# Kernel tuning notes

Measured on AMD Instinct MI355X. Metric: run time of the kernel, lower is better.

Reference implementation:

```python
import jax, jax.numpy as jnp
import numpy as np

N = 50000
E = 800000
IN_C = 128
HID = 64
HEADS = 4
OUT_C = 1
NEG_SLOPE = 0.2  # PyG GATConv default


def setup_inputs() -> dict:
    key = jax.random.key(0)
    ks = jax.random.split(key, 12)
    s = 1.0 / np.sqrt(IN_C)
    s2 = 1.0 / np.sqrt(HEADS * HID)
    return {
        "x": jax.random.normal(ks[0], (N, IN_C), jnp.float32),
        "edge_index": jax.random.randint(ks[1], (2, E), 0, N, jnp.int64),
        # layer 1 params (heads=HEADS, concat=True)
        "W1": jax.random.normal(ks[2], (IN_C, HEADS * HID), jnp.float32) * s,
        "att_src1": jax.random.normal(ks[3], (HEADS, HID), jnp.float32) * s,
        "att_dst1": jax.random.normal(ks[4], (HEADS, HID), jnp.float32) * s,
        "b1": jnp.zeros((HEADS * HID,), jnp.float32),
        # layer 2 params (heads=1, concat=False)
        "W2": jax.random.normal(ks[5], (HEADS * HID, OUT_C), jnp.float32) * s2,
        "att_src2": jax.random.normal(ks[6], (1, OUT_C), jnp.float32) * s2,
        "att_dst2": jax.random.normal(ks[7], (1, OUT_C), jnp.float32) * s2,
        "b2": jnp.zeros((OUT_C,), jnp.float32),
    }


def _gat_layer(x, src, dst, W, att_src, att_dst, b, concat):
    heads, out_c = att_src.shape
    h = (x @ W).reshape(-1, heads, out_c)          # [N, H, F]
    # per-node attention scores, gathered per edge (scalars, cheap)
    s_src = jnp.einsum('nhf,hf->nh', h, att_src)   # [N, H]
    s_dst = jnp.einsum('nhf,hf->nh', h, att_dst)
    e = jax.nn.leaky_relu(s_src[src] + s_dst[dst], NEG_SLOPE)  # [E, H]
    # segment softmax over edges sharing a destination
    m = jax.ops.segment_max(e, dst, num_segments=N)            # [N, H]
    m = jnp.where(jnp.isfinite(m), m, 0.0)
    ex = jnp.exp(e - m[dst])
    denom = jax.ops.segment_sum(ex, dst, num_segments=N)       # [N, H]
    alpha = ex / denom[dst]                                    # [E, H]
    # weighted scatter-aggregate of source features
    agg = jax.ops.segment_sum(alpha[:, :, None] * h[src], dst, num_segments=N)  # [N, H, F]
    out = agg.reshape(-1, heads * out_c) if concat else agg.mean(axis=1)
    return out + b


def reference(x, edge_index, W1, att_src1, att_dst1, b1, W2, att_src2, att_dst2, b2):
    # PyG GATConv default: add self loops
    loop = jnp.arange(N, dtype=edge_index.dtype)
    src = jnp.concatenate([edge_index[0], loop])
    dst = jnp.concatenate([edge_index[1], loop])
    h = _gat_layer(x, src, dst, W1, att_src1, att_dst1, b1, concat=True)
    h = jax.nn.elu(h)
    return _gat_layer(h, src, dst, W2, att_src2, att_dst2, b2, concat=False)
```

## Files before the change

kernel.cpp:

```cpp
#include <hip/hip_runtime.h>
#include <math.h>

#define NN 50000
#define EE 800000
#define ETOT 850000
#define NEG 0.2f
#define CAP 64

typedef unsigned short ushort_t;
typedef __attribute__((ext_vector_type(8))) short bf16x8;
typedef __attribute__((ext_vector_type(4))) float f32x4;

__device__ __forceinline__ float bf2f(ushort_t u) {
    return __uint_as_float((unsigned)u << 16);
}
__device__ __forceinline__ ushort_t f2bf(float f) {
    unsigned u = __float_as_uint(f);
    unsigned r = (u + 0x7FFFu + ((u >> 16) & 1u)) >> 16;
    return (ushort_t)r;
}

__global__ void k_detect(const void* ei, int* flag) {
    if (threadIdx.x == 0) {
        const long long* p = (const long long*)ei;
        int ok = 1;
        for (int i = 0; i < 64; ++i) {
            long long v = p[i];
            if (v < 0 || v >= NN) ok = 0;
        }
        *flag = ok;
    }
}

__device__ __forceinline__ int load_idx(const void* ei, int f64, long long pos) {
    return f64 ? (int)((const long long*)ei)[pos] : ((const int*)ei)[pos];
}

__global__ void k_fill(const void* ei, const int* __restrict__ flag,
                       int* cursor, int* __restrict__ esrc) {
    int e = blockIdx.x * blockDim.x + threadIdx.x;
    if (e >= ETOT) return;
    int f = *flag;
    int src, dst;
    if (e < EE) {
        src = load_idx(ei, f, e);
        dst = load_idx(ei, f, (long long)EE + e);
    } else {
        src = dst = e - EE;
    }
    int pos = atomicAdd(&cursor[dst], 1);
    if (pos < CAP) esrc[dst * CAP + pos] = src;
}

__global__ __launch_bounds__(256) void k_wprep(const float* __restrict__ W,
                                               ushort_t* __restrict__ Wf) {
    int idx = blockIdx.x * 256 + threadIdx.x;
    int e = idx & 7, l = (idx >> 3) & 63, ct = (idx >> 9) & 15, kt = idx >> 13;
    int k = kt * 32 + (l >> 4) * 8 + e;
    int col = ct * 16 + (l & 15);
    Wf[idx] = f2bf(W[k * 256 + col]);
}

__device__ __forceinline__ bf16x8 cvt8(float4 a, float4 b) {
    bf16x8 v;
    v[0] = (short)f2bf(a.x); v[1] = (short)f2bf(a.y);
    v[2] = (short)f2bf(a.z); v[3] = (short)f2bf(a.w);
    v[4] = (short)f2bf(b.x); v[5] = (short)f2bf(b.y);
    v[6] = (short)f2bf(b.z); v[7] = (short)f2bf(b.w);
    return v;
}

__global__ __launch_bounds__(256) void k_gemm_mfma(
    const float* __restrict__ x, const ushort_t* __restrict__ Wf,
    const float* __restrict__ aS, const float* __restrict__ aD,
    ushort_t* __restrict__ h1b, float* __restrict__ sS, float* __restrict__ sD) {
    int t = threadIdx.x, wid = t >> 6, l = t & 63;
    int lg = l >> 4, lr = l & 15;
    int r0 = blockIdx.x * 32;
    int c0 = wid * 64;
    int rowA0 = r0 + lr;       if (rowA0 >= NN) rowA0 = NN - 1;
    int rowA1 = r0 + 16 + lr;  if (rowA1 >= NN) rowA1 = NN - 1;
    const float4* X0 = (const float4*)(x + (size_t)rowA0 * 128) + lg * 2;
    const float4* X1 = (const float4*)(x + (size_t)rowA1 * 128) + lg * 2;
    const bf16x8* Bv = (const bf16x8*)Wf;

    f32x4 acc[2][4] = {};
#pragma unroll
    for (int kt = 0; kt < 4; ++kt) {
        bf16x8 a0 = cvt8(X0[kt * 8], X0[kt * 8 + 1]);
        bf16x8 a1 = cvt8(X1[kt * 8], X1[kt * 8 + 1]);
#pragma unroll
        for (int ct = 0; ct < 4; ++ct) {
            bf16x8 b = Bv[(size_t)((kt * 16 + wid * 4 + ct) * 64 + l)];
            acc[0][ct] = __builtin_amdgcn_mfma_f32_16x16x32_bf16(a0, b, acc[0][ct], 0, 0, 0);
            acc[1][ct] = __builtin_amdgcn_mfma_f32_16x16x32_bf16(a1, b, acc[1][ct], 0, 0, 0);
        }
    }
    float aSl[4], aDl[4];
#pragma unroll
    for (int ct = 0; ct < 4; ++ct) {
        aSl[ct] = aS[c0 + ct * 16 + lr];
        aDl[ct] = aD[c0 + ct * 16 + lr];
    }
#pragma unroll
    for (int rt = 0; rt < 2; ++rt) {
#pragma unroll
        for (int q = 0; q < 4; ++q) {
            int row = r0 + rt * 16 + lg * 4 + q;
            bool ok = row < NN;
            float p = 0.f, dd = 0.f;
#pragma unroll
            for (int ct = 0; ct < 4; ++ct) {
                float v = acc[rt][ct][q];
                if (ok) h1b[(size_t)row * 256 + c0 + ct * 16 + lr] = f2bf(v);
                p = fmaf(v, aSl[ct], p);
                dd = fmaf(v, aDl[ct], dd);
            }
#pragma unroll
            for (int k = 8; k >= 1; k >>= 1) {
                p += __shfl_xor(p, k, 64);
                dd += __shfl_xor(dd, k, 64);
            }
            if (ok && lr == 0) {
                sS[row * 4 + wid] = p;
                sD[row * 4 + wid] = dd;
            }
        }
    }
}

__global__ __launch_bounds__(256) void k_agg1(
    const int* __restrict__ cursor, const int* __restrict__ esrc,
    const ushort_t* __restrict__ h1b, const float* __restrict__ sS,
    const float* __restrict__ sD, const float* __restrict__ b1,
    const float* __restrict__ W2, float* __restrict__ g) {
    __shared__ float4 e_lds[4][CAP];
    __shared__ int s_lds[4][CAP];
    int wid = threadIdx.x >> 6, lane = threadIdx.x & 63;
    int n = blockIdx.x * 4 + wid;
    if (n >= NN) return;
    int d = cursor[n];
    if (d > CAP) d = CAP;
    int dp = (d + 3) & ~3;
    float sd0 = sD[n * 4 + 0], sd1 = sD[n * 4 + 1];
    float sd2 = sD[n * 4 + 2], sd3 = sD[n * 4 + 3];
    float e0 = -1e30f, e1 = -1e30f, e2 = -1e30f, e3 = -1e30f;
    int s = 0;
    if (lane < d) {
        s = esrc[n * CAP + lane];
        float4 ss = *(const float4*)(sS + (size_t)s * 4);
        e0 = ss.x + sd0; e0 = e0 > 0.f ? e0 : NEG * e0;
        e1 = ss.y + sd1; e1 = e1 > 0.f ? e1 : NEG * e1;
        e2 = ss.z + sd2; e2 = e2 > 0.f ? e2 : NEG * e2;
        e3 = ss.w + sd3; e3 = e3 > 0.f ? e3 : NEG * e3;
    }
    if (lane < dp) {
        e_lds[wid][lane] = make_float4(e0, e1, e2, e3);
        s_lds[wid][lane] = s;
    }
    float m0 = e0, m1 = e1, m2 = e2, m3 = e3;
#pragma unroll
    for (int k = 32; k >= 1; k >>= 1) {
        m0 = fmaxf(m0, __shfl_xor(m0, k, 64));
        m1 = fmaxf(m1, __shfl_xor(m1, k, 64));
        m2 = fmaxf(m2, __shfl_xor(m2, k, 64));
        m3 = fmaxf(m3, __shfl_xor(m3, k, 64));
    }
    float a0 = 0, a1 = 0, a2 = 0, a3 = 0;
    float d0 = 0, d1 = 0, d2 = 0, d3 = 0;
    for (int j = 0; j < dp; j += 4) {
        float4 ev0 = e_lds[wid][j + 0];
        float4 ev1 = e_lds[wid][j + 1];
        float4 ev2 = e_lds[wid][j + 2];
        float4 ev3 = e_lds[wid][j + 3];
        int s0 = s_lds[wid][j + 0];
        int s1 = s_lds[wid][j + 1];
        int s2 = s_lds[wid][j + 2];
        int s3 = s_lds[wid][j + 3];
        const ushort_t* h0 = h1b + (size_t)s0 * 256 + lane;
        const ushort_t* h1 = h1b + (size_t)s1 * 256 + lane;
        const ushort_t* h2 = h1b + (size_t)s2 * 256 + lane;
        const ushort_t* h3 = h1b + (size_t)s3 * 256 + lane;
        ushort_t u00 = h0[0], u01 = h0[64], u02 = h0[128], u03 = h0[192];
        ushort_t u10 = h1[0], u11 = h1[64], u12 = h1[128], u13 = h1[192];
        ushort_t u20 = h2[0], u21 = h2[64], u22 = h2[128], u23 = h2[192];
        ushort_t u30 = h3[0], u31 = h3[64], u32 = h3[128], u33 = h3[192];
        float x00 = __expf(ev0.x - m0), x01 = __expf(ev0.y - m1);
        float x02 = __expf(ev0.z - m2), x03 = __expf(ev0.w - m3);
        float x10 = __expf(ev1.x - m0), x11 = __expf(ev1.y - m1);
        float x12 = __expf(ev1.z - m2), x13 = __expf(ev1.w - m3);
        float x20 = __expf(ev2.x - m0), x21 = __expf(ev2.y - m1);
        float x22 = __expf(ev2.z - m2), x23 = __expf(ev2.w - m3);
        float x30 = __expf(ev3.x - m0), x31 = __expf(ev3.y - m1);
        float x32 = __expf(ev3.z - m2), x33 = __expf(ev3.w - m3);
        d0 += (x00 + x10) + (x20 + x30);
        d1 += (x01 + x11) + (x21 + x31);
        d2 += (x02 + x12) + (x22 + x32);
        d3 += (x03 + x13) + (x23 + x33);
        a0 = fmaf(x00, bf2f(u00), a0); a0 = fmaf(x10, bf2f(u10), a0);
        a0 = fmaf(x20, bf2f(u20), a0); a0 = fmaf(x30, bf2f(u30), a0);
        a1 = fmaf(x01, bf2f(u01), a1); a1 = fmaf(x11, bf2f(u11), a1);
        a1 = fmaf(x21, bf2f(u21), a1); a1 = fmaf(x31, bf2f(u31), a1);
        a2 = fmaf(x02, bf2f(u02), a2); a2 = fmaf(x12, bf2f(u12), a2);
        a2 = fmaf(x22, bf2f(u22), a2); a2 = fmaf(x32, bf2f(u32), a2);
        a3 = fmaf(x03, bf2f(u03), a3); a3 = fmaf(x13, bf2f(u13), a3);
        a3 = fmaf(x23, bf2f(u23), a3); a3 = fmaf(x33, bf2f(u33), a3);
    }
    float o0 = a0 / d0 + b1[lane];
    float o1 = a1 / d1 + b1[64 + lane];
    float o2 = a2 / d2 + b1[128 + lane];
    float o3 = a3 / d3 + b1[192 + lane];
    o0 = o0 > 0.f ? o0 : expm1f(o0);
    o1 = o1 > 0.f ? o1 : expm1f(o1);
    o2 = o2 > 0.f ? o2 : expm1f(o2);
    o3 = o3 > 0.f ? o3 : expm1f(o3);
    float part = o0 * W2[lane] + o1 * W2[64 + lane] + o2 * W2[128 + lane] + o3 * W2[192 + lane];
#pragma unroll
    for (int k = 32; k >= 1; k >>= 1) part += __shfl_xor(part, k, 64);
    if (lane == 0) g[n] = part;
}

__global__ __launch_bounds__(256) void k_layer2(
    const int* __restrict__ cursor, const int* __restrict__ esrc,
    const float* __restrict__ g, const float* __restrict__ aS2,
    const float* __restrict__ aD2, const float* __restrict__ b2,
    float* __restrict__ out) {
    int wid = threadIdx.x >> 6, lane = threadIdx.x & 63;
    int n = blockIdx.x * 4 + wid;
    if (n >= NN) return;
    int d = cursor[n];
    if (d > CAP) d = CAP;
    float aS = aS2[0], aD = aD2[0];
    float dn = g[n] * aD;
    float gv = 0.f, e = -1e30f;
    if (lane < d) {
        gv = g[esrc[n * CAP + lane]];
        e = gv * aS + dn;
        e = e > 0.f ? e : NEG * e;
    }
    float m = e;
#pragma unroll
    for (int k = 32; k >= 1; k >>= 1) m = fmaxf(m, __shfl_xor(m, k, 64));
    float ex = (lane < d) ? __expf(e - m) : 0.f;
    float den = ex, ws = ex * gv;
#pragma unroll
    for (int k = 32; k >= 1; k >>= 1) {
        den += __shfl_xor(den, k, 64);
        ws += __shfl_xor(ws, k, 64);
    }
    if (lane == 0) out[n] = ws / den + b2[0];
}

extern "C" void kernel_launch(void* const* d_in, const int* in_sizes, int n_in,
                              void* d_out, int out_size, void* d_ws, size_t ws_size,
                              hipStream_t stream) {
    const float* x   = (const float*)d_in[0];
    const void*  ei  = d_in[1];
    const float* W1  = (const float*)d_in[2];
    const float* aS1 = (const float*)d_in[3];
    const float* aD1 = (const float*)d_in[4];
    const float* b1  = (const float*)d_in[5];
    const float* W2  = (const float*)d_in[6];
    const float* aS2 = (const float*)d_in[7];
    const float* aD2 = (const float*)d_in[8];
    const float* b2  = (const float*)d_in[9];
    float* out = (float*)d_out;

    char* w = (char*)d_ws;
    size_t off = 0;
    auto take = [&](size_t bytes) {
        char* p = w + off;
        off = (off + bytes + 255) & ~(size_t)255;
        return p;
    };
    int*      flag   = (int*)take(4);
    int*      cursor = (int*)take((size_t)NN * 4);
    int*      esrc   = (int*)take((size_t)NN * CAP * 4);
    float*    sS     = (float*)take((size_t)NN * 4 * 4);
    float*    sD     = (float*)take((size_t)NN * 4 * 4);
    float*    g      = (float*)take((size_t)NN * 4);
    ushort_t* h1b    = (ushort_t*)take((size_t)NN * 256 * 2);
    ushort_t* Wf     = (ushort_t*)take((size_t)128 * 256 * 2);
    (void)ws_size; (void)in_sizes; (void)n_in; (void)out_size;

    hipMemsetAsync(cursor, 0, (size_t)NN * 4, stream);
    k_detect<<<1, 64, 0, stream>>>(ei, flag);
    k_fill<<<(ETOT + 255) / 256, 256, 0, stream>>>(ei, flag, cursor, esrc);
    k_wprep<<<128, 256, 0, stream>>>(W1, Wf);
    k_gemm_mfma<<<(NN + 31) / 32, 256, 0, stream>>>(x, W1 ? Wf : Wf, aS1, aD1, h1b, sS, sD);
    k_agg1<<<(NN + 3) / 4, 256, 0, stream>>>(cursor, esrc, h1b, sS, sD, b1, W2, g);
    k_layer2<<<(NN + 3) / 4, 256, 0, stream>>>(cursor, esrc, g, aS2, aD2, b2, out);
}
```

Baseline: 175.8 us.

## Pack h1 per-lane as uint2 and precompute softmax weights once per edge

The GEMM now writes h1 in a permuted layout where each lane holds four bf16 values (one per column tile) as a uint2, so the aggregation does one 8-byte gather per edge instead of four 2-byte gathers. Softmax normalisation moves out of the edge loop: alpha is computed once per edge via wave reductions and stored in LDS, removing 16 exps per iteration. Bias and W2 are pre-permuted to match the new layout, and the GEMM tile grows to 64 rows per block for more MFMA reuse of the B fragments, at the cost of more registers.

```diff
diff --git a/kernel.cpp b/kernel.cpp
--- a/kernel.cpp
+++ b/kernel.cpp
@@ -14,10 +14,9 @@
 __device__ __forceinline__ float bf2f(ushort_t u) {
     return __uint_as_float((unsigned)u << 16);
 }
-__device__ __forceinline__ ushort_t f2bf(float f) {
+__device__ __forceinline__ unsigned f2bf(float f) {
     unsigned u = __float_as_uint(f);
-    unsigned r = (u + 0x7FFFu + ((u >> 16) & 1u)) >> 16;
-    return (ushort_t)r;
+    return (u + 0x7FFFu + ((u >> 16) & 1u)) >> 16;
 }
 
 __global__ void k_detect(const void* ei, int* flag) {
@@ -53,12 +52,26 @@
 }
 
 __global__ __launch_bounds__(256) void k_wprep(const float* __restrict__ W,
-                                               ushort_t* __restrict__ Wf) {
+                                               const float* __restrict__ b1,
+                                               const float* __restrict__ W2,
+                                               ushort_t* __restrict__ Wf,
+                                               float* __restrict__ b1p,
+                                               float* __restrict__ W2p) {
     int idx = blockIdx.x * 256 + threadIdx.x;
-    int e = idx & 7, l = (idx >> 3) & 63, ct = (idx >> 9) & 15, kt = idx >> 13;
-    int k = kt * 32 + (l >> 4) * 8 + e;
-    int col = ct * 16 + (l & 15);
-    Wf[idx] = f2bf(W[k * 256 + col]);
+    if (idx < 32768) {
+        int e = idx & 7, l = (idx >> 3) & 63, ct = (idx >> 9) & 15, kt = idx >> 13;
+        int k = kt * 32 + (l >> 4) * 8 + e;
+        int col = ct * 16 + (l & 15);
+        Wf[idx] = (ushort_t)f2bf(W[k * 256 + col]);
+    } else if (idx < 32768 + 256) {
+        int c = idx - 32768;
+        int head = c >> 4, lrr = c & 15;
+#pragma unroll
+        for (int k = 0; k < 4; ++k) {
+            b1p[c * 4 + k] = b1[head * 64 + lrr + 16 * k];
+            W2p[c * 4 + k] = W2[head * 64 + lrr + 16 * k];
+        }
+    }
 }
 
 __device__ __forceinline__ bf16x8 cvt8(float4 a, float4 b) {
@@ -73,27 +86,32 @@
 __global__ __launch_bounds__(256) void k_gemm_mfma(
     const float* __restrict__ x, const ushort_t* __restrict__ Wf,
     const float* __restrict__ aS, const float* __restrict__ aD,
-    ushort_t* __restrict__ h1b, float* __restrict__ sS, float* __restrict__ sD) {
+    uint2* __restrict__ h1c, float* __restrict__ sS, float* __restrict__ sD) {
     int t = threadIdx.x, wid = t >> 6, l = t & 63;
     int lg = l >> 4, lr = l & 15;
-    int r0 = blockIdx.x * 32;
+    int r0 = blockIdx.x * 64;
     int c0 = wid * 64;
-    int rowA0 = r0 + lr;       if (rowA0 >= NN) rowA0 = NN - 1;
-    int rowA1 = r0 + 16 + lr;  if (rowA1 >= NN) rowA1 = NN - 1;
-    const float4* X0 = (const float4*)(x + (size_t)rowA0 * 128) + lg * 2;
-    const float4* X1 = (const float4*)(x + (size_t)rowA1 * 128) + lg * 2;
+    const float4* X[4];
+#pragma unroll
+    for (int rt = 0; rt < 4; ++rt) {
+        int r = r0 + rt * 16 + lr;
+        if (r >= NN) r = NN - 1;
+        X[rt] = (const float4*)(x + (size_t)r * 128) + lg * 2;
+    }
     const bf16x8* Bv = (const bf16x8*)Wf;
 
-    f32x4 acc[2][4] = {};
+    f32x4 acc[4][4] = {};
 #pragma unroll
     for (int kt = 0; kt < 4; ++kt) {
-        bf16x8 a0 = cvt8(X0[kt * 8], X0[kt * 8 + 1]);
-        bf16x8 a1 = cvt8(X1[kt * 8], X1[kt * 8 + 1]);
+        bf16x8 a[4];
+#pragma unroll
+        for (int rt = 0; rt < 4; ++rt) a[rt] = cvt8(X[rt][kt * 8], X[rt][kt * 8 + 1]);
 #pragma unroll
         for (int ct = 0; ct < 4; ++ct) {
             bf16x8 b = Bv[(size_t)((kt * 16 + wid * 4 + ct) * 64 + l)];
-            acc[0][ct] = __builtin_amdgcn_mfma_f32_16x16x32_bf16(a0, b, acc[0][ct], 0, 0, 0);
-            acc[1][ct] = __builtin_amdgcn_mfma_f32_16x16x32_bf16(a1, b, acc[1][ct], 0, 0, 0);
+#pragma unroll
+            for (int rt = 0; rt < 4; ++rt)
+                acc[rt][ct] = __builtin_amdgcn_mfma_f32_16x16x32_bf16(a[rt], b, acc[rt][ct], 0, 0, 0);
         }
     }
     float aSl[4], aDl[4];
@@ -103,19 +121,19 @@
         aDl[ct] = aD[c0 + ct * 16 + lr];
     }
 #pragma unroll
-    for (int rt = 0; rt < 2; ++rt) {
+    for (int rt = 0; rt < 4; ++rt) {
 #pragma unroll
         for (int q = 0; q < 4; ++q) {
             int row = r0 + rt * 16 + lg * 4 + q;
             bool ok = row < NN;
-            float p = 0.f, dd = 0.f;
-#pragma unroll
-            for (int ct = 0; ct < 4; ++ct) {
-                float v = acc[rt][ct][q];
-                if (ok) h1b[(size_t)row * 256 + c0 + ct * 16 + lr] = f2bf(v);
-                p = fmaf(v, aSl[ct], p);
-                dd = fmaf(v, aDl[ct], dd);
-            }
+            float v0 = acc[rt][0][q], v1 = acc[rt][1][q];
+            float v2 = acc[rt][2][q], v3 = acc[rt][3][q];
+            float p = v0 * aSl[0] + v1 * aSl[1] + v2 * aSl[2] + v3 * aSl[3];
+            float dd = v0 * aDl[0] + v1 * aDl[1] + v2 * aDl[2] + v3 * aDl[3];
+            uint2 u;
+            u.x = (f2bf(v1) << 16) | f2bf(v0);
+            u.y = (f2bf(v3) << 16) | f2bf(v2);
+            if (ok) h1c[(size_t)row * 64 + wid * 16 + lr] = u;
 #pragma unroll
             for (int k = 8; k >= 1; k >>= 1) {
                 p += __shfl_xor(p, k, 64);
@@ -131,10 +149,10 @@
 
 __global__ __launch_bounds__(256) void k_agg1(
     const int* __restrict__ cursor, const int* __restrict__ esrc,
-    const ushort_t* __restrict__ h1b, const float* __restrict__ sS,
-    const float* __restrict__ sD, const float* __restrict__ b1,
-    const float* __restrict__ W2, float* __restrict__ g) {
-    __shared__ float4 e_lds[4][CAP];
+    const uint2* __restrict__ h1c, const float* __restrict__ sS,
+    const float* __restrict__ sD, const float* __restrict__ b1p,
+    const float* __restrict__ W2p, float* __restrict__ g) {
+    __shared__ float al_lds[4][CAP][4];
     __shared__ int s_lds[4][CAP];
     int wid = threadIdx.x >> 6, lane = threadIdx.x & 63;
     int n = blockIdx.x * 4 + wid;
@@ -142,21 +160,16 @@
     int d = cursor[n];
     if (d > CAP) d = CAP;
     int dp = (d + 3) & ~3;
-    float sd0 = sD[n * 4 + 0], sd1 = sD[n * 4 + 1];
-    float sd2 = sD[n * 4 + 2], sd3 = sD[n * 4 + 3];
+    float4 sd = *(const float4*)(sD + (size_t)n * 4);
     float e0 = -1e30f, e1 = -1e30f, e2 = -1e30f, e3 = -1e30f;
     int s = 0;
     if (lane < d) {
         s = esrc[n * CAP + lane];
         float4 ss = *(const float4*)(sS + (size_t)s * 4);
-        e0 = ss.x + sd0; e0 = e0 > 0.f ? e0 : NEG * e0;
-        e1 = ss.y + sd1; e1 = e1 > 0.f ? e1 : NEG * e1;
-        e2 = ss.z + sd2; e2 = e2 > 0.f ? e2 : NEG * e2;
-        e3 = ss.w + sd3; e3 = e3 > 0.f ? e3 : NEG * e3;
-    }
-    if (lane < dp) {
-        e_lds[wid][lane] = make_float4(e0, e1, e2, e3);
-        s_lds[wid][lane] = s;
+        e0 = ss.x + sd.x; e0 = e0 > 0.f ? e0 : NEG * e0;
+        e1 = ss.y + sd.y; e1 = e1 > 0.f ? e1 : NEG * e1;
+        e2 = ss.z + sd.z; e2 = e2 > 0.f ? e2 : NEG * e2;
+        e3 = ss.w + sd.w; e3 = e3 > 0.f ? e3 : NEG * e3;
     }
     float m0 = e0, m1 = e1, m2 = e2, m3 = e3;
 #pragma unroll
@@ -166,55 +179,68 @@
         m2 = fmaxf(m2, __shfl_xor(m2, k, 64));
         m3 = fmaxf(m3, __shfl_xor(m3, k, 64));
     }
-    float a0 = 0, a1 = 0, a2 = 0, a3 = 0;
-    float d0 = 0, d1 = 0, d2 = 0, d3 = 0;
+    float x0 = __expf(e0 - m0);
+    float x1 = __expf(e1 - m1);
+    float x2 = __expf(e2 - m2);
+    float x3 = __expf(e3 - m3);
+    float q0 = x0, q1 = x1, q2 = x2, q3 = x3;
+#pragma unroll
+    for (int k = 32; k >= 1; k >>= 1) {
+        q0 += __shfl_xor(q0, k, 64);
+        q1 += __shfl_xor(q1, k, 64);
+        q2 += __shfl_xor(q2, k, 64);
+        q3 += __shfl_xor(q3, k, 64);
+    }
+    if (lane < dp) {
+        al_lds[wid][lane][0] = x0 / q0;
+        al_lds[wid][lane][1] = x1 / q1;
+        al_lds[wid][lane][2] = x2 / q2;
+        al_lds[wid][lane][3] = x3 / q3;
+        s_lds[wid][lane] = s;
+    }
+    int hsel = lane >> 4;
+    float a0 = 0.f, a1 = 0.f, a2 = 0.f, a3 = 0.f;
     for (int j = 0; j < dp; j += 4) {
-        float4 ev0 = e_lds[wid][j + 0];
-        float4 ev1 = e_lds[wid][j + 1];
-        float4 ev2 = e_lds[wid][j + 2];
-        float4 ev3 = e_lds[wid][j + 3];
         int s0 = s_lds[wid][j + 0];
         int s1 = s_lds[wid][j + 1];
         int s2 = s_lds[wid][j + 2];
         int s3 = s_lds[wid][j + 3];
-        const ushort_t* h0 = h1b + (size_t)s0 * 256 + lane;
-        const ushort_t* h1 = h1b + (size_t)s1 * 256 + lane;
-        const ushort_t* h2 = h1b + (size_t)s2 * 256 + lane;
-        const ushort_t* h3 = h1b + (size_t)s3 * 256 + lane;
-        ushort_t u00 = h0[0], u01 = h0[64], u02 = h0[128], u03 = h0[192];
-        ushort_t u10 = h1[0], u11 = h1[64], u12 = h1[128], u13 = h1[192];
-        ushort_t u20 = h2[0], u21 = h2[64], u22 = h2[128], u23 = h2[192];
-        ushort_t u30 = h3[0], u31 = h3[64], u32 = h3[128], u33 = h3[192];
-        float x00 = __expf(ev0.x - m0), x01 = __expf(ev0.y - m1);
-        float x02 = __expf(ev0.z - m2), x03 = __expf(ev0.w - m3);
-        float x10 = __expf(ev1.x - m0), x11 = __expf(ev1.y - m1);
-        float x12 = __expf(ev1.z - m2), x13 = __expf(ev1.w - m3);
-        float x20 = __expf(ev2.x - m0), x21 = __expf(ev2.y - m1);
-        float x22 = __expf(ev2.z - m2), x23 = __expf(ev2.w - m3);
-        float x30 = __expf(ev3.x - m0), x31 = __expf(ev3.y - m1);
-        float x32 = __expf(ev3.z - m2), x33 = __expf(ev3.w - m3);
-        d0 += (x00 + x10) + (x20 + x30);
-        d1 += (x01 + x11) + (x21 + x31);
-        d2 += (x02 + x12) + (x22 + x32);
-        d3 += (x03 + x13) + (x23 + x33);
-        a0 = fmaf(x00, bf2f(u00), a0); a0 = fmaf(x10, bf2f(u10), a0);
-        a0 = fmaf(x20, bf2f(u20), a0); a0 = fmaf(x30, bf2f(u30), a0);
-        a1 = fmaf(x01, bf2f(u01), a1); a1 = fmaf(x11, bf2f(u11), a1);
-        a1 = fmaf(x21, bf2f(u21), a1); a1 = fmaf(x31, bf2f(u31), a1);
-        a2 = fmaf(x02, bf2f(u02), a2); a2 = fmaf(x12, bf2f(u12), a2);
-        a2 = fmaf(x22, bf2f(u22), a2); a2 = fmaf(x32, bf2f(u32), a2);
-        a3 = fmaf(x03, bf2f(u03), a3); a3 = fmaf(x13, bf2f(u13), a3);
-        a3 = fmaf(x23, bf2f(u23), a3); a3 = fmaf(x33, bf2f(u33), a3);
-    }
-    float o0 = a0 / d0 + b1[lane];
-    float o1 = a1 / d1 + b1[64 + lane];
-    float o2 = a2 / d2 + b1[128 + lane];
-    float o3 = a3 / d3 + b1[192 + lane];
+        float w0 = al_lds[wid][j + 0][hsel];
+        float w1 = al_lds[wid][j + 1][hsel];
+        float w2 = al_lds[wid][j + 2][hsel];
+        float w3 = al_lds[wid][j + 3][hsel];
+        uint2 u0 = h1c[(size_t)s0 * 64 + lane];
+        uint2 u1 = h1c[(size_t)s1 * 64 + lane];
+        uint2 u2 = h1c[(size_t)s2 * 64 + lane];
+        uint2 u3 = h1c[(size_t)s3 * 64 + lane];
+        a0 = fmaf(w0, __uint_as_float(u0.x << 16), a0);
+        a1 = fmaf(w0, __uint_as_float(u0.x & 0xffff0000u), a1);
+        a2 = fmaf(w0, __uint_as_float(u0.y << 16), a2);
+        a3 = fmaf(w0, __uint_as_float(u0.y & 0xffff0000u), a3);
+        a0 = fmaf(w1, __uint_as_float(u1.x << 16), a0);
+        a1 = fmaf(w1, __uint_as_float(u1.x & 0xffff0000u), a1);
+        a2 = fmaf(w1, __uint_as_float(u1.y << 16), a2);
+        a3 = fmaf(w1, __uint_as_float(u1.y & 0xffff0000u), a3);
+        a0 = fmaf(w2, __uint_as_float(u2.x << 16), a0);
+        a1 = fmaf(w2, __uint_as_float(u2.x & 0xffff0000u), a1);
+        a2 = fmaf(w2, __uint_as_float(u2.y << 16), a2);
+        a3 = fmaf(w2, __uint_as_float(u2.y & 0xffff0000u), a3);
+        a0 = fmaf(w3, __uint_as_float(u3.x << 16), a0);
+        a1 = fmaf(w3, __uint_as_float(u3.x & 0xffff0000u), a1);
+        a2 = fmaf(w3, __uint_as_float(u3.y << 16), a2);
+        a3 = fmaf(w3, __uint_as_float(u3.y & 0xffff0000u), a3);
+    }
+    float4 bv = ((const float4*)b1p)[lane];
+    float4 wv = ((const float4*)W2p)[lane];
+    float o0 = a0 + bv.x;
+    float o1 = a1 + bv.y;
+    float o2 = a2 + bv.z;
+    float o3 = a3 + bv.w;
     o0 = o0 > 0.f ? o0 : expm1f(o0);
     o1 = o1 > 0.f ? o1 : expm1f(o1);
     o2 = o2 > 0.f ? o2 : expm1f(o2);
     o3 = o3 > 0.f ? o3 : expm1f(o3);
-    float part = o0 * W2[lane] + o1 * W2[64 + lane] + o2 * W2[128 + lane] + o3 * W2[192 + lane];
+    float part = o0 * wv.x + o1 * wv.y + o2 * wv.z + o3 * wv.w;
 #pragma unroll
     for (int k = 32; k >= 1; k >>= 1) part += __shfl_xor(part, k, 64);
     if (lane == 0) g[n] = part;
@@ -279,15 +305,17 @@
     float*    sS     = (float*)take((size_t)NN * 4 * 4);
     float*    sD     = (float*)take((size_t)NN * 4 * 4);
     float*    g      = (float*)take((size_t)NN * 4);
-    ushort_t* h1b    = (ushort_t*)take((size_t)NN * 256 * 2);
+    uint2*    h1c    = (uint2*)take((size_t)NN * 64 * 8);
     ushort_t* Wf     = (ushort_t*)take((size_t)128 * 256 * 2);
+    float*    b1p    = (float*)take((size_t)256 * 4 * 4);
+    float*    W2p    = (float*)take((size_t)256 * 4 * 4);
     (void)ws_size; (void)in_sizes; (void)n_in; (void)out_size;
 
     hipMemsetAsync(cursor, 0, (size_t)NN * 4, stream);
     k_detect<<<1, 64, 0, stream>>>(ei, flag);
     k_fill<<<(ETOT + 255) / 256, 256, 0, stream>>>(ei, flag, cursor, esrc);
-    k_wprep<<<128, 256, 0, stream>>>(W1, Wf);
-    k_gemm_mfma<<<(NN + 31) / 32, 256, 0, stream>>>(x, W1 ? Wf : Wf, aS1, aD1, h1b, sS, sD);
-    k_agg1<<<(NN + 3) / 4, 256, 0, stream>>>(cursor, esrc, h1b, sS, sD, b1, W2, g);
+    k_wprep<<<129, 256, 0, stream>>>(W1, b1, W2, Wf, b1p, W2p);
+    k_gemm_mfma<<<(NN + 63) / 64, 256, 0, stream>>>(x, Wf, aS1, aD1, h1c, sS, sD);
+    k_agg1<<<(NN + 3) / 4, 256, 0, stream>>>(cursor, esrc, h1c, sS, sD, b1p, W2p, g);
     k_layer2<<<(NN + 3) / 4, 256, 0, stream>>>(cursor, esrc, g, aS2, aD2, b2, out);
 }
```

Result: no change. 177.6 us (+1.0%).
